# Kernel optimization log

Measured on AMD Instinct MI355X. Metric: run time of the kernel, lower is better.

## Reference

```python
import jax, jax.numpy as jnp
import numpy as np

N_HEADS = 4

def _conv2d(x, w, b):
    # NCHW input, OIHW weight, 3x3 SAME, stride 1
    y = jax.lax.conv_general_dilated(x, w, window_strides=(1, 1), padding='SAME',
                                     dimension_numbers=('NCHW', 'OIHW', 'NCHW'))
    return y + b[None, :, None, None]


def setup_inputs() -> dict:
    key = jax.random.key(0)
    ks = jax.random.split(key, 5)
    x = jax.random.normal(ks[0], (4, 32, 256, 256), dtype=jnp.float32)
    conv1_w = jax.random.normal(ks[1], (384, 32, 3, 3), dtype=jnp.float32) * 0.05
    conv1_b = jax.random.normal(ks[2], (384,), dtype=jnp.float32) * 0.05
    conv2_w = jax.random.normal(ks[3], (32, 128, 3, 3), dtype=jnp.float32) * 0.05
    conv2_b = jax.random.normal(ks[4], (32,), dtype=jnp.float32) * 0.05
    return {'x': x, 'conv1_w': conv1_w, 'conv1_b': conv1_b,
            'conv2_w': conv2_w, 'conv2_b': conv2_b}


def reference(x, conv1_w, conv1_b, conv2_w, conv2_b):
    b, c_in, h, w = x.shape
    n = h * w
    qkv = _conv2d(x, conv1_w, conv1_b)              # [b, 3*heads*d, h, w]
    d = qkv.shape[1] // (3 * N_HEADS)               # head dim
    qkv = qkv.reshape(b, 3, N_HEADS, d, n)          # 'b (qkv heads c) h w -> b qkv heads c n'
    q, k, v = qkv[:, 0], qkv[:, 1], qkv[:, 2]
    k = jax.nn.softmax(k, axis=-1)                  # softmax over n = h*w
    weights = jnp.einsum('bhdn,bhen->bhde', q, k)   # [b, heads, d, d] context
    out = jnp.einsum('bhde,bhdn->bhen', weights, v) # [b, heads, d, n]
    out = out.reshape(b, N_HEADS * d, h, w)         # 'b heads c n -> b (heads c) h w'
    return _conv2d(out, conv2_w, conv2_b)
```

## Files before the change

### kernel.cpp

```cpp
#include <hip/hip_runtime.h>
#include <hip/hip_bf16.h>

typedef __hip_bfloat16 bf16;
typedef __attribute__((ext_vector_type(8))) short short8;
typedef __attribute__((ext_vector_type(4))) float f32x4;
typedef __attribute__((ext_vector_type(16))) float f32x16;

#define B_    4
#define CIN   32
#define HH    256
#define WW    256
#define C1    384
#define NPIX  65536
#define CMID  128
#define COUT  32
#define PW    258

static __device__ __forceinline__ float u2f(unsigned short u) {
    unsigned int x = ((unsigned int)u) << 16;
    return __uint_as_float(x);
}
static __device__ __forceinline__ unsigned short f2u(float f) {
    bf16 h = __float2bfloat16(f);
    return __builtin_bit_cast(unsigned short, h);
}
static __device__ __forceinline__ unsigned int pk2(float lo, float hi) {
    return (unsigned int)f2u(lo) | ((unsigned int)f2u(hi) << 16);
}
static __device__ __forceinline__ void gload16(const void* src, void* dst) {
    __builtin_amdgcn_global_load_lds(
        (const __attribute__((address_space(1))) void*)src,
        (__attribute__((address_space(3))) void*)dst, 16, 0, 0);
}

__global__ __launch_bounds__(256) void k_w1t(const float* __restrict__ w1, short* __restrict__ w1t) {
    const int tap = blockIdx.x;
    for (int i = threadIdx.x; i < 384 * 32; i += 256) {
        int co = i >> 5, cij = i & 31;
        w1t[((size_t)(tap * 4 + (cij >> 3)) * 384 + co) * 8 + (cij & 7)] =
            (short)f2u(w1[(size_t)i * 9 + tap]);
    }
}
__global__ __launch_bounds__(256) void k_w2t(const float* __restrict__ w2, short* __restrict__ w2t) {
    const int tap = blockIdx.x;
    for (int i = threadIdx.x; i < 32 * 128; i += 256) {
        int co = i >> 7, cij = i & 127;
        w2t[((size_t)(tap * 16 + (cij >> 3)) * 32 + co) * 8 + (cij & 7)] =
            (short)f2u(w2[(size_t)i * 9 + tap]);
    }
}

__global__ __launch_bounds__(256) void k_xt2(const float* __restrict__ x,
                                             unsigned short* __restrict__ xt2, int b0) {
    const int row = blockIdx.x, bl = blockIdx.y, b = b0 + bl;
    const int tx = threadIdx.x;
    unsigned short* rbase = xt2 + (size_t)(bl * PW + row) * 4 * PW * 8;
    const uint4 z = make_uint4(0u, 0u, 0u, 0u);
    if (row == 0 || row == PW - 1) {
        for (int i = tx; i < 4 * PW; i += 256) ((uint4*)rbase)[i] = z;
        return;
    }
    if (tx < 2) {
        int c = tx ? (PW - 1) : 0;
#pragma unroll
        for (int ch = 0; ch < 4; ch++)
            *(uint4*)(rbase + ((size_t)ch * PW + c) * 8) = z;
    }
    const int col = tx + 1;
    const size_t px = (size_t)(row - 1) * WW + tx;
    unsigned int pk[16];
#pragma unroll
    for (int c2 = 0; c2 < 16; c2++) {
        float v0 = x[((size_t)b * CIN + 2 * c2) * NPIX + px];
        float v1 = x[((size_t)b * CIN + 2 * c2 + 1) * NPIX + px];
        pk[c2] = pk2(v0, v1);
    }
#pragma unroll
    for (int ch = 0; ch < 4; ch++)
        *(uint4*)(rbase + ((size_t)ch * PW + col) * 8) =
            make_uint4(pk[ch * 4], pk[ch * 4 + 1], pk[ch * 4 + 2], pk[ch * 4 + 3]);
}

__global__ __launch_bounds__(256, 3) void k_conv1(
    const unsigned short* __restrict__ xt2, const short* __restrict__ w1t,
    const float* __restrict__ b1, unsigned short* __restrict__ vt,
    float* __restrict__ pw, float* __restrict__ ps, int nb)
{
    const int nblk = 512 * nb;
    const int m = ((int)blockIdx.x & 7) * (nblk >> 3) + ((int)blockIdx.x >> 3);
    const int chunk = m & 1;
    const int y   = (m >> 1) & 255;
    const int bl  = m >> 9;
    const int px0 = chunk * 128;
    const int cid = bl * 512 + y * 2 + chunk;
    const int tx  = threadIdx.x;
    const int wv  = tx >> 6, l = tx & 63;
    const int lhi = l >> 4, llo = l & 15;

    __shared__ short xs[12 * 132 * 8];
    __shared__ union {
        short os[64][136];
        short ost[128][66];
        float osw[4][32][32];
    } ou;

#pragma unroll
    for (int i = 0; i < 3; i++) {
        int p = wv * 3 + i;
        int r = p >> 2, ch = p & 3;
        const char* src = (const char*)xt2 +
            (((size_t)(bl * PW) + y + r) * 4 + ch) * (PW * 16) + (size_t)px0 * 16 + (size_t)l * 16;
        char* dst = (char*)xs + p * 2112;
        gload16(src, dst);
        gload16(src + 1024, dst + 1024);
        if (l < 2) gload16(src + 2048, dst + 2048);
    }
    __syncthreads();

    const short* wbase = w1t + ((size_t)lhi * 384 + llo) * 8;

    short8 qa[2][4];
    f32x4 wacc[2][2];
#pragma unroll
    for (int dt = 0; dt < 2; dt++)
#pragma unroll
        for (int et = 0; et < 2; et++) wacc[dt][et] = (f32x4){0.f, 0.f, 0.f, 0.f};
    float se0 = 0.f, se1 = 0.f;

#pragma unroll
    for (int cog = 0; cog < 6; cog++) {
        const int co0 = cog * 64;

        f32x4 acc[2][4];
#pragma unroll
        for (int t = 0; t < 2; t++)
#pragma unroll
            for (int mc = 0; mc < 4; mc++) acc[t][mc] = (f32x4){0.f, 0.f, 0.f, 0.f};

        short8 a[4], an[4];
#pragma unroll
        for (int mc = 0; mc < 4; mc++)
            an[mc] = *(const short8*)(wbase + ((size_t)co0 + mc * 16) * 8);
#pragma unroll
        for (int tap = 0; tap < 9; tap++) {
            const int dy = tap / 3, dx = tap % 3;
#pragma unroll
            for (int mc = 0; mc < 4; mc++) a[mc] = an[mc];
            if (tap < 8) {
#pragma unroll
                for (int mc = 0; mc < 4; mc++)
                    an[mc] = *(const short8*)(wbase +
                        ((size_t)(tap + 1) * 4 * 384 + co0 + mc * 16) * 8);
            }
#pragma unroll
            for (int t = 0; t < 2; t++) {
                short8 bfr = *(const short8*)&xs[(((dy * 4 + lhi) * 132) + (wv * 32 + t * 16 + llo + dx)) * 8];
#pragma unroll
                for (int mc = 0; mc < 4; mc++)
                    acc[t][mc] = __builtin_amdgcn_mfma_f32_16x16x32_bf16(a[mc], bfr, acc[t][mc], 0, 0, 0);
            }
        }

        float bias[4][4];
#pragma unroll
        for (int mc = 0; mc < 4; mc++)
#pragma unroll
            for (int r = 0; r < 4; r++)
                bias[mc][r] = b1[co0 + mc * 16 + lhi * 4 + r];

        __syncthreads();

        if (cog < 4) {
#pragma unroll
            for (int t = 0; t < 2; t++)
#pragma unroll
                for (int mc = 0; mc < 4; mc++)
#pragma unroll
                    for (int r = 0; r < 4; r++)
                        ou.os[mc * 16 + lhi * 4 + r][wv * 32 + t * 16 + llo] =
                            (short)f2u(acc[t][mc][r] + bias[mc][r]);
        } else {
#pragma unroll
            for (int t = 0; t < 2; t++)
#pragma unroll
                for (int mc = 0; mc < 4; mc++)
#pragma unroll
                    for (int r = 0; r < 4; r++)
                        ou.ost[wv * 32 + t * 16 + llo][mc * 16 + lhi * 4 + r] =
                            (short)f2u(acc[t][mc][r] + bias[mc][r]);
        }
        __syncthreads();

        if (cog < 2) {
            if ((wv >> 1) == cog) {
                const int chb = (wv & 1) * 32;
#pragma unroll
                for (int dt = 0; dt < 2; dt++)
#pragma unroll
                    for (int ks = 0; ks < 4; ks++)
                        qa[dt][ks] = *(const short8*)&ou.os[chb + dt * 16 + llo][ks * 32 + lhi * 8];
            }
        } else if (cog < 4) {
            if ((wv >> 1) == cog - 2) {
                const int chb = (wv & 1) * 32;
#pragma unroll
                for (int et = 0; et < 2; et++)
#pragma unroll
                    for (int ks = 0; ks < 4; ks++) {
                        short8 kf = *(const short8*)&ou.os[chb + et * 16 + llo][ks * 32 + lhi * 8];
                        short8 pf;
#pragma unroll
                        for (int j = 0; j < 8; j++) {
                            float ef = __expf(u2f((unsigned short)kf[j]));
                            if (et == 0) se0 += ef; else se1 += ef;
                            pf[j] = (short)f2u(ef);
                        }
#pragma unroll
                        for (int dt = 0; dt < 2; dt++)
                            wacc[dt][et] = __builtin_amdgcn_mfma_f32_16x16x32_bf16(
                                qa[dt][ks], pf, wacc[dt][et], 0, 0, 0);
                    }
            }
        } else {
            unsigned short* dst = vt + ((size_t)(bl * 2 + (cog - 4)) * NPIX
                                        + y * WW + px0) * 64;
#pragma unroll
            for (int i = 0; i < 4; i++) {
                int u = i * 256 + tx;
                int px = u >> 3, q = u & 7;
                uint4 v = *(const uint4*)&ou.ost[px][q * 8];
                *(uint4*)(dst + (size_t)u * 8) = v;
            }
        }
    }

    se0 += __shfl_xor(se0, 16); se0 += __shfl_xor(se0, 32);
    se1 += __shfl_xor(se1, 16); se1 += __shfl_xor(se1, 32);
    if (l < 16) {
        ps[(size_t)cid * 128 + wv * 32 + llo]      = se0;
        ps[(size_t)cid * 128 + wv * 32 + 16 + llo] = se1;
    }

    __syncthreads();
#pragma unroll
    for (int dt = 0; dt < 2; dt++)
#pragma unroll
        for (int et = 0; et < 2; et++)
#pragma unroll
            for (int r = 0; r < 4; r++)
                ou.osw[wv][dt * 16 + lhi * 4 + r][et * 16 + llo] = wacc[dt][et][r];
    __syncthreads();

    {
        float* pwp = pw + (size_t)cid * 4096;
        const float* osf = (const float*)&ou;
#pragma unroll
        for (int p = 0; p < 4; p++)
            *(float4*)(pwp + p * 1024 + tx * 4) = *(const float4*)(osf + p * 1024 + tx * 4);
    }
}

__global__ __launch_bounds__(256) void k_wred(
    const float* __restrict__ pw, const float* __restrict__ ps,
    float* __restrict__ wts, int b0)
{
    const int bh = blockIdx.x;
    const int jq = blockIdx.y;
    const int bl = bh >> 2, h = bh & 3;
    const int tx = threadIdx.x;
    __shared__ float rinvs[32];
    if (tx < 32) {
        float s = 0.f;
        const float* pp = ps + (size_t)bl * 512 * 128 + h * 32 + tx;
        for (int c = 0; c < 512; c++) s += pp[(size_t)c * 128];
        rinvs[tx] = 1.f / s;
    }
    __syncthreads();
    const int i = jq * 256 + tx;
    const float* pwp = pw + (size_t)bl * 512 * 4096 + h * 1024 + i;
    float s = 0.f;
    for (int c = 0; c < 512; c++) s += pwp[(size_t)c * 4096];
    wts[(size_t)(b0 * 4 + bh) * 1024 + i] = s * rinvs[i & 31];
}

__global__ __launch_bounds__(256) void k_bord(unsigned short* __restrict__ at2) {
    const int row = blockIdx.x, bl = blockIdx.y, tx = threadIdx.x;
    unsigned short* base = at2 + (size_t)(bl * PW + row) * 16 * PW * 8;
    const uint4 z = make_uint4(0u, 0u, 0u, 0u);
    if (row == 0 || row == PW - 1) {
        for (int i = tx; i < 16 * PW; i += 256) ((uint4*)base)[i] = z;
    } else if (tx < 32) {
        int g = tx >> 1, c = (tx & 1) * (PW - 1);
        *(uint4*)(base + ((size_t)g * PW + c) * 8) = z;
    }
}

__global__ __launch_bounds__(256, 4) void k_attnout(
    const unsigned short* __restrict__ vt, const float* __restrict__ wts,
    unsigned short* __restrict__ at2, int b0, int nb)
{
    const int bl = blockIdx.y, b = b0 + bl;
    const int tx = threadIdx.x, wv = tx >> 6, l = tx & 63;
    const int e = l & 31, kg = l >> 5;
    const int pxb = blockIdx.x * 256 + wv * 64;

    __shared__ float osa[4][32][34];

    short8 Bf[4][2];
    const float* Wb = wts + (size_t)b * 4096;
#pragma unroll
    for (int h = 0; h < 4; h++)
#pragma unroll
        for (int kk = 0; kk < 2; kk++) {
            short8 v;
#pragma unroll
            for (int j = 0; j < 8; j++) {
                int d = kk * 16 + kg * 8 + j;
                v[j] = (short)f2u(Wb[h * 1024 + d * 32 + e]);
            }
            Bf[h][kk] = v;
        }

    const unsigned short* vbase = vt + (size_t)bl * 2 * NPIX * 64;

#pragma unroll
    for (int t = 0; t < 2; t++) {
        const int px0 = pxb + t * 32;
#pragma unroll
        for (int h = 0; h < 4; h++) {
            const unsigned short* vp = vbase + (size_t)(h >> 1) * NPIX * 64
                                     + (size_t)(px0 + e) * 64 + (h & 1) * 32 + kg * 8;
            short8 a0 = *(const short8*)vp;
            short8 a1 = *(const short8*)(vp + 16);
            f32x16 acc;
#pragma unroll
            for (int r = 0; r < 16; r++) acc[r] = 0.f;
            acc = __builtin_amdgcn_mfma_f32_32x32x16_bf16(a0, Bf[h][0], acc, 0, 0, 0);
            acc = __builtin_amdgcn_mfma_f32_32x32x16_bf16(a1, Bf[h][1], acc, 0, 0, 0);

#pragma unroll
            for (int r = 0; r < 16; r++) {
                int pxl = (r & 3) + 8 * (r >> 2) + 4 * kg;
                osa[wv][e][pxl] = acc[r];
            }
#pragma unroll
            for (int it = 0; it < 2; it++) {
                int u = it * 64 + l;
                int eg = u >> 5, px = u & 31;
                short8 o;
#pragma unroll
                for (int j = 0; j < 8; j++) o[j] = (short)f2u(osa[wv][eg * 8 + j][px]);
                int gp = px0 + px;
                int prow = gp >> 8, pcol = gp & 255;
                *(short8*)(at2 + (((size_t)(bl * PW) + 1 + prow) * 16 + h * 4 + eg) * (PW * 8)
                           + (size_t)(1 + pcol) * 8) = o;
            }
        }
    }
}

__global__ __launch_bounds__(256, 3) void k_conv2(
    const unsigned short* __restrict__ at2, const short* __restrict__ w2t,
    const float* __restrict__ b2, float* __restrict__ out, int b0, int nb)
{
    const int bid = blockIdx.x;
    const int chunk = bid & 1;
    const int y   = (bid >> 1) & 255;
    const int bl  = bid >> 9;
    const int px0 = chunk * 128;
    const int bb  = b0 + bl;
    const int tx  = threadIdx.x;
    const int wv  = tx >> 6, l = tx & 63;
    const int lhi = l >> 4, llo = l & 15;

    __shared__ short xs[12 * 132 * 8];
    __shared__ float osf[32][132];

    float bias[2][4];
#pragma unroll
    for (int m = 0; m < 2; m++)
#pragma unroll
        for (int r = 0; r < 4; r++)
            bias[m][r] = b2[m * 16 + lhi * 4 + r];

    f32x4 acc[2][2];
#pragma unroll
    for (int t = 0; t < 2; t++)
#pragma unroll
        for (int m = 0; m < 2; m++) acc[t][m] = (f32x4){0.f, 0.f, 0.f, 0.f};

    for (int cc = 0; cc < 4; cc++) {
        __syncthreads();
#pragma unroll
        for (int i = 0; i < 3; i++) {
            int p = wv * 3 + i;
            int r = p >> 2, ch = p & 3;
            const char* src = (const char*)at2 +
                (((size_t)(bl * PW) + y + r) * 16 + cc * 4 + ch) * (PW * 16)
                + (size_t)px0 * 16 + (size_t)l * 16;
            char* dst = (char*)xs + p * 2112;
            gload16(src, dst);
            gload16(src + 1024, dst + 1024);
            if (l < 2) gload16(src + 2048, dst + 2048);
        }
        __syncthreads();

        short8 a[2], an[2];
#pragma unroll
        for (int m = 0; m < 2; m++)
            an[m] = *(const short8*)(w2t + ((size_t)(cc * 4 + lhi) * 32 + m * 16 + llo) * 8);
#pragma unroll
        for (int tap = 0; tap < 9; tap++) {
            const int dy = tap / 3, dx = tap % 3;
#pragma unroll
            for (int m = 0; m < 2; m++) a[m] = an[m];
            if (tap < 8) {
#pragma unroll
                for (int m = 0; m < 2; m++)
                    an[m] = *(const short8*)(w2t +
                        ((size_t)((tap + 1) * 16 + cc * 4 + lhi) * 32 + m * 16 + llo) * 8);
            }
#pragma unroll
            for (int t = 0; t < 2; t++) {
                short8 bfr = *(const short8*)&xs[(((dy * 4 + lhi) * 132) + (wv * 32 + t * 16 + llo + dx)) * 8];
#pragma unroll
                for (int m = 0; m < 2; m++)
                    acc[t][m] = __builtin_amdgcn_mfma_f32_16x16x32_bf16(a[m], bfr, acc[t][m], 0, 0, 0);
            }
        }
    }

#pragma unroll
    for (int t = 0; t < 2; t++)
#pragma unroll
        for (int m = 0; m < 2; m++)
#pragma unroll
            for (int r = 0; r < 4; r++)
                osf[m * 16 + lhi * 4 + r][wv * 32 + t * 16 + llo] = acc[t][m][r] + bias[m][r];
    __syncthreads();
#pragma unroll
    for (int p = 0; p < 4; p++) {
        int chl = p * 8 + (tx >> 5);
        float4 v = *(const float4*)&osf[chl][(tx & 31) * 4];
        *(float4*)(out + ((size_t)bb * COUT + chl) * NPIX + y * WW + px0 + (tx & 31) * 4) = v;
    }
}

extern "C" void kernel_launch(void* const* d_in, const int* in_sizes, int n_in,
                              void* d_out, int out_size, void* d_ws, size_t ws_size,
                              hipStream_t stream) {
    const float* x  = (const float*)d_in[0];
    const float* w1 = (const float*)d_in[1];
    const float* b1 = (const float*)d_in[2];
    const float* w2 = (const float*)d_in[3];
    const float* b2 = (const float*)d_in[4];
    float* out = (float*)d_out;

    char* ws = (char*)d_ws;
    float* wts  = (float*)(ws + 4096);
    short* w1t  = (short*)(ws + 69632);
    short* w2t  = (short*)(ws + 290816);
    const size_t OFF_XT = 1048576;

    int nb = 4;
    size_t xt_sz = (size_t)nb * PW * 4 * PW * 16;
    size_t pw_sz = (size_t)nb * 512 * 4096 * 4;
    size_t ps_sz = (size_t)nb * 512 * 128 * 4;
    size_t vt_sz = (size_t)nb * 2 * NPIX * 64 * 2;
    size_t at_sz = (size_t)nb * PW * PW * 256;
    if (ws_size < OFF_XT + xt_sz + pw_sz + ps_sz + vt_sz + at_sz) {
        nb = 1;
        xt_sz = (size_t)nb * PW * 4 * PW * 16;
        pw_sz = (size_t)nb * 512 * 4096 * 4;
        ps_sz = (size_t)nb * 512 * 128 * 4;
        vt_sz = (size_t)nb * 2 * NPIX * 64 * 2;
        at_sz = (size_t)nb * PW * PW * 256;
    }
    const size_t pw_off = OFF_XT + xt_sz;
    const size_t ps_off = pw_off + pw_sz;
    const size_t vt_off = ps_off + ps_sz;
    const size_t at_off = vt_off + vt_sz;

    unsigned short* xt2 = (unsigned short*)(ws + OFF_XT);
    float*          pw  = (float*)(ws + pw_off);
    float*          psb = (float*)(ws + ps_off);
    unsigned short* vt  = (unsigned short*)(ws + vt_off);
    unsigned short* at2 = (unsigned short*)(ws + at_off);

    k_w1t<<<dim3(9), 256, 0, stream>>>(w1, w1t);
    k_w2t<<<dim3(9), 256, 0, stream>>>(w2, w2t);

    for (int b0 = 0; b0 < B_; b0 += nb) {
        k_xt2    <<<dim3(PW, nb),        256, 0, stream>>>(x, xt2, b0);
        k_conv1  <<<dim3(2 * HH * nb),   256, 0, stream>>>(xt2, w1t, b1, vt, pw, psb, nb);
        k_wred   <<<dim3(nb * 4, 4),     256, 0, stream>>>(pw, psb, wts, b0);
        k_bord   <<<dim3(PW, nb),        256, 0, stream>>>(at2);
        k_attnout<<<dim3(NPIX / 256, nb),256, 0, stream>>>(vt, wts, at2, b0, nb);
        k_conv2  <<<dim3(2 * HH * nb),   256, 0, stream>>>(at2, w2t, b2, out, b0, nb);
    }
}
```

Before: 222.8 us.

## Fuse attention-output matmul into conv2, recomputing halo tiles in shared memory

Removes the separate border-zeroing and attention-output kernels and the padded intermediate buffer. The conv2 kernel now computes the weights-times-V product for its 3-row, halo-extended tile directly into shared memory, zeroing out-of-range pixels, then runs the 3x3 conv from there. This saves a full write and read of the bf16 intermediate and two launches, at the cost of recomputing halo rows (about 3x the attention MFMA work) and extra synchronisation per channel chunk. It also adds a block-index swizzle across the grid.

```diff
diff --git a/kernel.cpp b/kernel.cpp
--- a/kernel.cpp
+++ b/kernel.cpp
@@ -283,160 +283,127 @@
     wts[(size_t)(b0 * 4 + bh) * 1024 + i] = s * rinvs[i & 31];
 }
 
-__global__ __launch_bounds__(256) void k_bord(unsigned short* __restrict__ at2) {
-    const int row = blockIdx.x, bl = blockIdx.y, tx = threadIdx.x;
-    unsigned short* base = at2 + (size_t)(bl * PW + row) * 16 * PW * 8;
-    const uint4 z = make_uint4(0u, 0u, 0u, 0u);
-    if (row == 0 || row == PW - 1) {
-        for (int i = tx; i < 16 * PW; i += 256) ((uint4*)base)[i] = z;
-    } else if (tx < 32) {
-        int g = tx >> 1, c = (tx & 1) * (PW - 1);
-        *(uint4*)(base + ((size_t)g * PW + c) * 8) = z;
-    }
-}
-
-__global__ __launch_bounds__(256, 4) void k_attnout(
-    const unsigned short* __restrict__ vt, const float* __restrict__ wts,
-    unsigned short* __restrict__ at2, int b0, int nb)
+__global__ __launch_bounds__(256, 3) void k_conv2f(
+    const unsigned short* __restrict__ vt, const short* __restrict__ w2t,
+    const float* __restrict__ wts, const float* __restrict__ b2,
+    float* __restrict__ out, int b0, int nb)
 {
-    const int bl = blockIdx.y, b = b0 + bl;
-    const int tx = threadIdx.x, wv = tx >> 6, l = tx & 63;
-    const int e = l & 31, kg = l >> 5;
-    const int pxb = blockIdx.x * 256 + wv * 64;
-
-    __shared__ float osa[4][32][34];
-
-    short8 Bf[4][2];
-    const float* Wb = wts + (size_t)b * 4096;
-#pragma unroll
-    for (int h = 0; h < 4; h++)
-#pragma unroll
-        for (int kk = 0; kk < 2; kk++) {
-            short8 v;
-#pragma unroll
-            for (int j = 0; j < 8; j++) {
-                int d = kk * 16 + kg * 8 + j;
-                v[j] = (short)f2u(Wb[h * 1024 + d * 32 + e]);
-            }
-            Bf[h][kk] = v;
-        }
-
-    const unsigned short* vbase = vt + (size_t)bl * 2 * NPIX * 64;
-
-#pragma unroll
-    for (int t = 0; t < 2; t++) {
-        const int px0 = pxb + t * 32;
-#pragma unroll
-        for (int h = 0; h < 4; h++) {
-            const unsigned short* vp = vbase + (size_t)(h >> 1) * NPIX * 64
-                                     + (size_t)(px0 + e) * 64 + (h & 1) * 32 + kg * 8;
-            short8 a0 = *(const short8*)vp;
-            short8 a1 = *(const short8*)(vp + 16);
-            f32x16 acc;
-#pragma unroll
-            for (int r = 0; r < 16; r++) acc[r] = 0.f;
-            acc = __builtin_amdgcn_mfma_f32_32x32x16_bf16(a0, Bf[h][0], acc, 0, 0, 0);
-            acc = __builtin_amdgcn_mfma_f32_32x32x16_bf16(a1, Bf[h][1], acc, 0, 0, 0);
-
-#pragma unroll
-            for (int r = 0; r < 16; r++) {
-                int pxl = (r & 3) + 8 * (r >> 2) + 4 * kg;
-                osa[wv][e][pxl] = acc[r];
-            }
-#pragma unroll
-            for (int it = 0; it < 2; it++) {
-                int u = it * 64 + l;
-                int eg = u >> 5, px = u & 31;
-                short8 o;
-#pragma unroll
-                for (int j = 0; j < 8; j++) o[j] = (short)f2u(osa[wv][eg * 8 + j][px]);
-                int gp = px0 + px;
-                int prow = gp >> 8, pcol = gp & 255;
-                *(short8*)(at2 + (((size_t)(bl * PW) + 1 + prow) * 16 + h * 4 + eg) * (PW * 8)
-                           + (size_t)(1 + pcol) * 8) = o;
-            }
-        }
-    }
-}
-
-__global__ __launch_bounds__(256, 3) void k_conv2(
-    const unsigned short* __restrict__ at2, const short* __restrict__ w2t,
-    const float* __restrict__ b2, float* __restrict__ out, int b0, int nb)
-{
-    const int bid = blockIdx.x;
-    const int chunk = bid & 1;
-    const int y   = (bid >> 1) & 255;
-    const int bl  = bid >> 9;
+    const int nblk = 512 * nb;
+    const int m = ((int)blockIdx.x & 7) * (nblk >> 3) + ((int)blockIdx.x >> 3);
+    const int chunk = m & 1;
+    const int y   = (m >> 1) & 255;
+    const int bl  = m >> 9;
     const int px0 = chunk * 128;
     const int bb  = b0 + bl;
     const int tx  = threadIdx.x;
     const int wv  = tx >> 6, l = tx & 63;
     const int lhi = l >> 4, llo = l & 15;
 
-    __shared__ short xs[12 * 132 * 8];
+    __shared__ short xs[12 * 137 * 8];
     __shared__ float osf[32][132];
+    __shared__ short wtsb[4][2][64][8];
+
+    for (int i = tx; i < 4096; i += 256) {
+        int h = i >> 10, r = i & 1023;
+        int kh = r >> 9, s = r & 511, li = s >> 3, j = s & 7;
+        int d = kh * 16 + (li >> 5) * 8 + j, e = li & 31;
+        wtsb[h][kh][li][j] = (short)f2u(wts[(size_t)bb * 4096 + h * 1024 + d * 32 + e]);
+    }
 
     float bias[2][4];
 #pragma unroll
-    for (int m = 0; m < 2; m++)
+    for (int mm = 0; mm < 2; mm++)
 #pragma unroll
         for (int r = 0; r < 4; r++)
-            bias[m][r] = b2[m * 16 + lhi * 4 + r];
+            bias[mm][r] = b2[mm * 16 + lhi * 4 + r];
 
     f32x4 acc[2][2];
 #pragma unroll
     for (int t = 0; t < 2; t++)
 #pragma unroll
-        for (int m = 0; m < 2; m++) acc[t][m] = (f32x4){0.f, 0.f, 0.f, 0.f};
+        for (int mm = 0; mm < 2; mm++) acc[t][mm] = (f32x4){0.f, 0.f, 0.f, 0.f};
+
+    __syncthreads();
+
+    const int kg = l >> 5;
+    const int pxa = l & 31;
 
     for (int cc = 0; cc < 4; cc++) {
-        __syncthreads();
-#pragma unroll
-        for (int i = 0; i < 3; i++) {
-            int p = wv * 3 + i;
-            int r = p >> 2, ch = p & 3;
-            const char* src = (const char*)at2 +
-                (((size_t)(bl * PW) + y + r) * 16 + cc * 4 + ch) * (PW * 16)
-                + (size_t)px0 * 16 + (size_t)l * 16;
-            char* dst = (char*)xs + p * 2112;
-            gload16(src, dst);
-            gload16(src + 1024, dst + 1024);
-            if (l < 2) gload16(src + 2048, dst + 2048);
+        const int plane = cc >> 1, chofs = (cc & 1) * 32;
+        short8 B0 = *(const short8*)&wtsb[cc][0][l][0];
+        short8 B1 = *(const short8*)&wtsb[cc][1][l][0];
+
+        for (int idx = wv; idx < 15; idx += 4) {
+            int rr = idx / 5, ti = idx % 5;
+            int ar = y - 1 + rr;
+            int colbase = (ti < 4) ? ti * 32 : 99;
+            if (ar < 0 || ar > 255) {
+#pragma unroll
+                for (int r = 0; r < 16; r++) {
+                    int pxl = (r & 3) + 8 * (r >> 2) + 4 * kg;
+                    int e = pxa;
+                    xs[(((rr * 4 + (e >> 3)) * 137) + colbase + pxl) * 8 + (e & 7)] = 0;
+                }
+            } else {
+                int ac = px0 - 1 + colbase + pxa;
+                short8 A0 = (short8){0,0,0,0,0,0,0,0};
+                short8 A1 = (short8){0,0,0,0,0,0,0,0};
+                if (ac >= 0 && ac < 256) {
+                    const unsigned short* vp = vt +
+                        ((size_t)(bl * 2 + plane) * NPIX + (size_t)ar * 256 + ac) * 64
+                        + chofs + kg * 8;
+                    A0 = *(const short8*)vp;
+                    A1 = *(const short8*)(vp + 16);
+                }
+                f32x16 aa;
+#pragma unroll
+                for (int r = 0; r < 16; r++) aa[r] = 0.f;
+                aa = __builtin_amdgcn_mfma_f32_32x32x16_bf16(A0, B0, aa, 0, 0, 0);
+                aa = __builtin_amdgcn_mfma_f32_32x32x16_bf16(A1, B1, aa, 0, 0, 0);
+#pragma unroll
+                for (int r = 0; r < 16; r++) {
+                    int pxl = (r & 3) + 8 * (r >> 2) + 4 * kg;
+                    int e = pxa;
+                    xs[(((rr * 4 + (e >> 3)) * 137) + colbase + pxl) * 8 + (e & 7)] =
+                        (short)f2u(aa[r]);
+                }
+            }
         }
         __syncthreads();
 
         short8 a[2], an[2];
 #pragma unroll
-        for (int m = 0; m < 2; m++)
-            an[m] = *(const short8*)(w2t + ((size_t)(cc * 4 + lhi) * 32 + m * 16 + llo) * 8);
+        for (int mm = 0; mm < 2; mm++)
+            an[mm] = *(const short8*)(w2t + ((size_t)(cc * 4 + lhi) * 32 + mm * 16 + llo) * 8);
 #pragma unroll
         for (int tap = 0; tap < 9; tap++) {
             const int dy = tap / 3, dx = tap % 3;
 #pragma unroll
-            for (int m = 0; m < 2; m++) a[m] = an[m];
+            for (int mm = 0; mm < 2; mm++) a[mm] = an[mm];
             if (tap < 8) {
 #pragma unroll
-                for (int m = 0; m < 2; m++)
-                    an[m] = *(const short8*)(w2t +
-                        ((size_t)((tap + 1) * 16 + cc * 4 + lhi) * 32 + m * 16 + llo) * 8);
+                for (int mm = 0; mm < 2; mm++)
+                    an[mm] = *(const short8*)(w2t +
+                        ((size_t)((tap + 1) * 16 + cc * 4 + lhi) * 32 + mm * 16 + llo) * 8);
             }
 #pragma unroll
             for (int t = 0; t < 2; t++) {
-                short8 bfr = *(const short8*)&xs[(((dy * 4 + lhi) * 132) + (wv * 32 + t * 16 + llo + dx)) * 8];
-#pragma unroll
-                for (int m = 0; m < 2; m++)
-                    acc[t][m] = __builtin_amdgcn_mfma_f32_16x16x32_bf16(a[m], bfr, acc[t][m], 0, 0, 0);
+                short8 bfr = *(const short8*)&xs[(((dy * 4 + lhi) * 137) + (wv * 32 + t * 16 + llo + dx)) * 8];
+#pragma unroll
+                for (int mm = 0; mm < 2; mm++)
+                    acc[t][mm] = __builtin_amdgcn_mfma_f32_16x16x32_bf16(a[mm], bfr, acc[t][mm], 0, 0, 0);
             }
         }
+        __syncthreads();
     }
 
 #pragma unroll
     for (int t = 0; t < 2; t++)
 #pragma unroll
-        for (int m = 0; m < 2; m++)
+        for (int mm = 0; mm < 2; mm++)
 #pragma unroll
             for (int r = 0; r < 4; r++)
-                osf[m * 16 + lhi * 4 + r][wv * 32 + t * 16 + llo] = acc[t][m][r] + bias[m][r];
+                osf[mm * 16 + lhi * 4 + r][wv * 32 + t * 16 + llo] = acc[t][mm][r] + bias[mm][r];
     __syncthreads();
 #pragma unroll
     for (int p = 0; p < 4; p++) {
@@ -467,35 +434,29 @@
     size_t pw_sz = (size_t)nb * 512 * 4096 * 4;
     size_t ps_sz = (size_t)nb * 512 * 128 * 4;
     size_t vt_sz = (size_t)nb * 2 * NPIX * 64 * 2;
-    size_t at_sz = (size_t)nb * PW * PW * 256;
-    if (ws_size < OFF_XT + xt_sz + pw_sz + ps_sz + vt_sz + at_sz) {
+    if (ws_size < OFF_XT + xt_sz + pw_sz + ps_sz + vt_sz) {
         nb = 1;
         xt_sz = (size_t)nb * PW * 4 * PW * 16;
         pw_sz = (size_t)nb * 512 * 4096 * 4;
         ps_sz = (size_t)nb * 512 * 128 * 4;
         vt_sz = (size_t)nb * 2 * NPIX * 64 * 2;
-        at_sz = (size_t)nb * PW * PW * 256;
     }
     const size_t pw_off = OFF_XT + xt_sz;
     const size_t ps_off = pw_off + pw_sz;
     const size_t vt_off = ps_off + ps_sz;
-    const size_t at_off = vt_off + vt_sz;
 
     unsigned short* xt2 = (unsigned short*)(ws + OFF_XT);
     float*          pw  = (float*)(ws + pw_off);
     float*          psb = (float*)(ws + ps_off);
     unsigned short* vt  = (unsigned short*)(ws + vt_off);
-    unsigned short* at2 = (unsigned short*)(ws + at_off);
 
     k_w1t<<<dim3(9), 256, 0, stream>>>(w1, w1t);
     k_w2t<<<dim3(9), 256, 0, stream>>>(w2, w2t);
 
     for (int b0 = 0; b0 < B_; b0 += nb) {
-        k_xt2    <<<dim3(PW, nb),        256, 0, stream>>>(x, xt2, b0);
-        k_conv1  <<<dim3(2 * HH * nb),   256, 0, stream>>>(xt2, w1t, b1, vt, pw, psb, nb);
-        k_wred   <<<dim3(nb * 4, 4),     256, 0, stream>>>(pw, psb, wts, b0);
-        k_bord   <<<dim3(PW, nb),        256, 0, stream>>>(at2);
-        k_attnout<<<dim3(NPIX / 256, nb),256, 0, stream>>>(vt, wts, at2, b0, nb);
-        k_conv2  <<<dim3(2 * HH * nb),   256, 0, stream>>>(at2, w2t, b2, out, b0, nb);
-    }
-}
+        k_xt2  <<<dim3(PW, nb),      256, 0, stream>>>(x, xt2, b0);
+        k_conv1<<<dim3(2 * HH * nb), 256, 0, stream>>>(xt2, w1t, b1, vt, pw, psb, nb);
+        k_wred <<<dim3(nb * 4, 4),   256, 0, stream>>>(pw, psb, wts, b0);
+        k_conv2f<<<dim3(2 * HH * nb),256, 0, stream>>>(vt, w2t, wts, b2, out, b0, nb);
+    }
+}
```

Measured after the change: 197.0 us. -11.6%, faster.
